# Kernel tuning notes

Hardware: AMD Instinct MI355X
Metric: run time of the kernel (lower is better)

The kernel has to match this reference:

```python
import jax, jax.numpy as jnp
import numpy as np

N_NODES = 100000


def gcn_conv(x, edge_index, W, b, n):
    """PyG GCNConv: h = x @ W; add self-loops; symmetric deg^-1/2 norm; scatter-add; + bias."""
    h = x @ W  # [N, out] -- transform first (PyG order), small message dim
    src, dst = edge_index[0], edge_index[1]
    loop = jnp.arange(n, dtype=src.dtype)
    src = jnp.concatenate([src, loop])
    dst = jnp.concatenate([dst, loop])
    # degree over targets with unit edge weights (includes self-loops)
    deg = jax.ops.segment_sum(jnp.ones_like(src, dtype=h.dtype), dst, num_segments=n)
    dinv = jnp.where(deg > 0, deg ** -0.5, 0.0)
    norm = dinv[src] * dinv[dst]  # [E+N]
    msg = h[src] * norm[:, None]  # gather + scale
    out = jax.ops.segment_sum(msg, dst, num_segments=n)  # scatter-add aggregate
    return out + b


def setup_inputs() -> dict:
    key = jax.random.key(0)
    k1, k2, k3, k4, k5, k6 = jax.random.split(key, 6)
    input_dim, hidden_dim, output_dim = 128, 16, 2
    x = jax.random.normal(k1, (N_NODES, input_dim), dtype=jnp.float32)
    edge_index = jax.random.randint(k2, (2, 3200000), 0, N_NODES, dtype=jnp.int64)
    s1 = (1.0 / np.sqrt(input_dim)).astype(np.float32)
    s2 = (1.0 / np.sqrt(hidden_dim)).astype(np.float32)
    W1 = jax.random.normal(k3, (input_dim, hidden_dim), dtype=jnp.float32) * s1
    b1 = jnp.zeros((hidden_dim,), dtype=jnp.float32)
    W2 = jax.random.normal(k4, (hidden_dim, output_dim), dtype=jnp.float32) * s2
    b2 = jnp.zeros((output_dim,), dtype=jnp.float32)
    return {"x": x, "edge_index": edge_index, "W1": W1, "b1": b1, "W2": W2, "b2": b2}


def reference(x, edge_index, W1, b1, W2, b2):
    n = x.shape[0]
    h = gcn_conv(x, edge_index, W1, b1, n)
    h = jax.nn.relu(h)
    out = gcn_conv(h, edge_index, W2, b2, n)
    return out
```

## Files before the change

### kernel.cpp

```cpp
#include <hip/hip_runtime.h>
#include <hip/hip_fp16.h>
#include <math.h>

constexpr int F_IN   = 128;
constexpr int F_H    = 16;
constexpr int F_OUT  = 2;
constexpr int BSH    = 8;
constexpr int BNODES = 1 << BSH;
constexpr int MAXB   = 512;
constexpr int BIN_SPAN = 8192;
constexpr int CAP    = 12288;

__global__ __launch_bounds__(256) void bcount_kernel(const int* __restrict__ dst, int E,
                                                     int* __restrict__ bcnt, int NB) {
    __shared__ int h[MAXB];
    for (int i = threadIdx.x; i < MAXB; i += 256) h[i] = 0;
    __syncthreads();
    int stride = gridDim.x * 256;
    for (int e = blockIdx.x * 256 + threadIdx.x; e < E; e += stride)
        atomicAdd(&h[dst[e] >> BSH], 1);
    __syncthreads();
    for (int b = threadIdx.x; b < NB; b += 256) {
        int c = h[b];
        if (c) atomicAdd(&bcnt[b], c);
    }
}

__global__ __launch_bounds__(256) void bscan_kernel(const int* __restrict__ bcnt,
                                                    int* __restrict__ boff,
                                                    int* __restrict__ gcur, int NB, int E) {
    __shared__ int warp_s[4];
    int t = threadIdx.x;
    int base = t * 4;
    int v0 = (base + 0 < NB) ? bcnt[base + 0] : 0;
    int v1 = (base + 1 < NB) ? bcnt[base + 1] : 0;
    int v2 = (base + 2 < NB) ? bcnt[base + 2] : 0;
    int v3 = (base + 3 < NB) ? bcnt[base + 3] : 0;
    int tsum = v0 + v1 + v2 + v3;
    int lane = t & 63, wid = t >> 6;
    int x = tsum;
    for (int d = 1; d < 64; d <<= 1) {
        int y = __shfl_up(x, d, 64);
        if (lane >= d) x += y;
    }
    if (lane == 63) warp_s[wid] = x;
    __syncthreads();
    if (t == 0) {
        int a = 0;
        for (int w = 0; w < 4; ++w) { int s = warp_s[w]; warp_s[w] = a; a += s; }
    }
    __syncthreads();
    int excl = x - tsum + warp_s[wid];
    int p0 = excl, p1 = excl + v0, p2 = excl + v0 + v1, p3 = excl + v0 + v1 + v2;
    if (base + 0 < NB) { boff[base + 0] = p0; gcur[base + 0] = p0; }
    if (base + 1 < NB) { boff[base + 1] = p1; gcur[base + 1] = p1; }
    if (base + 2 < NB) { boff[base + 2] = p2; gcur[base + 2] = p2; }
    if (base + 3 < NB) { boff[base + 3] = p3; gcur[base + 3] = p3; }
    if (t == 0) boff[NB] = E;
}

__global__ __launch_bounds__(1024) void bin_kernel(const int* __restrict__ src,
                                                   const int* __restrict__ dst,
                                                   int* __restrict__ gcur,
                                                   int* __restrict__ ebuf, int E) {
    __shared__ int cnt[MAXB];
    __shared__ int loff[MAXB];
    __shared__ int gbase[MAXB];
    __shared__ int warp_s[MAXB / 64];
    __shared__ int stagep[BIN_SPAN];
    __shared__ unsigned short stageb[BIN_SPAN];
    int tid = threadIdx.x;
    for (int i = tid; i < MAXB; i += 1024) cnt[i] = 0;
    __syncthreads();
    int e0 = blockIdx.x * BIN_SPAN;
    int e1 = min(e0 + BIN_SPAN, E);
    int m = e1 - e0;
    for (int i = tid; i < m; i += 1024)
        atomicAdd(&cnt[dst[e0 + i] >> BSH], 1);
    __syncthreads();
    int v = 0, x = 0;
    int lane = tid & 63, wid = tid >> 6;
    if (tid < MAXB) {
        v = cnt[tid];
        x = v;
        for (int d = 1; d < 64; d <<= 1) {
            int y = __shfl_up(x, d, 64);
            if (lane >= d) x += y;
        }
        if (lane == 63) warp_s[wid] = x;
    }
    __syncthreads();
    if (tid == 0) {
        int a = 0;
        for (int w = 0; w < MAXB / 64; ++w) { int s = warp_s[w]; warp_s[w] = a; a += s; }
    }
    __syncthreads();
    if (tid < MAXB) {
        int lo = x - v + warp_s[wid];
        loff[tid] = lo;
        gbase[tid] = (v ? atomicAdd(&gcur[tid], v) : 0) - lo;
        cnt[tid] = 0;
    }
    __syncthreads();
    for (int i = tid; i < m; i += 1024) {
        int d = dst[e0 + i];
        int b = d >> BSH;
        int r = atomicAdd(&cnt[b], 1);
        int idx = loff[b] + r;
        stagep[idx] = src[e0 + i] | ((d & (BNODES - 1)) << 17);
        stageb[idx] = (unsigned short)b;
    }
    __syncthreads();
    for (int i = tid; i < m; i += 1024)
        ebuf[gbase[stageb[i]] + i] = stagep[i];
}

__global__ __launch_bounds__(512) void csc_kernel(const int* __restrict__ boff,
                                                  int* __restrict__ ebuf,
                                                  float* __restrict__ dinv,
                                                  int* __restrict__ noff, int N) {
    __shared__ int stage[CAP];
    __shared__ int cnt[BNODES];
    __shared__ int loff[BNODES];
    __shared__ int cur[BNODES];
    int tid = threadIdx.x;
    int b = blockIdx.x;
    if (tid < BNODES) cnt[tid] = 0;
    __syncthreads();
    int e0 = boff[b], e1 = boff[b + 1];
    int m = min(e1 - e0, CAP);
    for (int i = tid; i < m; i += 512) {
        int v = ebuf[e0 + i];
        stage[i] = v;
        atomicAdd(&cnt[v >> 17], 1);
    }
    __syncthreads();
    if (tid == 0) {
        int a = 0;
        for (int j = 0; j < BNODES; ++j) { loff[j] = a; a += cnt[j]; }
    }
    __syncthreads();
    int n0 = b << BSH;
    if (tid < BNODES) {
        int node = n0 + tid;
        if (node < N) {
            dinv[node] = 1.0f / sqrtf((float)(cnt[tid] + 1));
            noff[node] = e0 + loff[tid];
        }
        cur[tid] = loff[tid];
    }
    if (tid == 0 && b == gridDim.x - 1) noff[N] = e1;
    __syncthreads();
    for (int i = tid; i < m; i += 512) {
        int v = stage[i];
        int p = atomicAdd(&cur[v >> 17], 1);
        ebuf[e0 + p] = v & 0x1FFFF;
    }
}

__global__ void gemm1_kernel(const float* __restrict__ x, const float* __restrict__ W1,
                             const float* __restrict__ dinv, __half* __restrict__ g1, int N) {
    __shared__ float w[F_IN * F_H];
    for (int t = threadIdx.x; t < F_IN * F_H; t += blockDim.x) w[t] = W1[t];
    __syncthreads();
    int row = blockIdx.x * blockDim.x + threadIdx.x;
    if (row >= N) return;
    float acc[F_H];
#pragma unroll
    for (int j = 0; j < F_H; ++j) acc[j] = 0.0f;
    const float4* xr = (const float4*)(x + (size_t)row * F_IN);
#pragma unroll 4
    for (int k4 = 0; k4 < F_IN / 4; ++k4) {
        float4 v = xr[k4];
        const float* wr = &w[k4 * 4 * F_H];
#pragma unroll
        for (int j = 0; j < F_H; ++j)
            acc[j] += v.x * wr[j] + v.y * wr[F_H + j] + v.z * wr[2 * F_H + j] + v.w * wr[3 * F_H + j];
    }
    float di = dinv[row];
    __half2 hh[8];
#pragma unroll
    for (int j = 0; j < 8; ++j)
        hh[j] = __floats2half2_rn(acc[2 * j] * di, acc[2 * j + 1] * di);
    uint4* gr = (uint4*)(g1 + (size_t)row * F_H);
    gr[0] = ((uint4*)hh)[0];
    gr[1] = ((uint4*)hh)[1];
}

__global__ __launch_bounds__(512) void agg1_kernel(
        const int* __restrict__ noff, const int* __restrict__ ebuf,
        const float* __restrict__ dinv, const __half2* __restrict__ g1,
        const float* __restrict__ b1, const float* __restrict__ W2,
        float* __restrict__ g2, int N) {
    int t = blockIdx.x * 512 + threadIdx.x;
    int node = t >> 3, lane = t & 7;
    if (node >= N) return;
    int k = noff[node], end = noff[node + 1];
    float2 a0 = make_float2(0.f, 0.f), a1 = a0, a2 = a0, a3 = a0;
    for (; k + 8 <= end; k += 8) {
        int s0 = ebuf[k + 0], s1 = ebuf[k + 1];
        int s2 = ebuf[k + 2], s3 = ebuf[k + 3];
        int s4 = ebuf[k + 4], s5 = ebuf[k + 5];
        int s6 = ebuf[k + 6], s7 = ebuf[k + 7];
        float2 v0 = __half22float2(g1[(s0 << 3) + lane]);
        float2 v1 = __half22float2(g1[(s1 << 3) + lane]);
        float2 v2 = __half22float2(g1[(s2 << 3) + lane]);
        float2 v3 = __half22float2(g1[(s3 << 3) + lane]);
        float2 v4 = __half22float2(g1[(s4 << 3) + lane]);
        float2 v5 = __half22float2(g1[(s5 << 3) + lane]);
        float2 v6 = __half22float2(g1[(s6 << 3) + lane]);
        float2 v7 = __half22float2(g1[(s7 << 3) + lane]);
        a0.x += v0.x; a0.y += v0.y;  a1.x += v1.x; a1.y += v1.y;
        a2.x += v2.x; a2.y += v2.y;  a3.x += v3.x; a3.y += v3.y;
        a0.x += v4.x; a0.y += v4.y;  a1.x += v5.x; a1.y += v5.y;
        a2.x += v6.x; a2.y += v6.y;  a3.x += v7.x; a3.y += v7.y;
    }
    for (; k < end; ++k) {
        float2 v = __half22float2(g1[(ebuf[k] << 3) + lane]);
        a0.x += v.x; a0.y += v.y;
    }
    float di = dinv[node];
    float2 sf = __half22float2(g1[(node << 3) + lane]);
    float sx = (a0.x + a1.x) + (a2.x + a3.x) + sf.x;
    float sy = (a0.y + a1.y) + (a2.y + a3.y) + sf.y;
    int j0 = 2 * lane, j1 = 2 * lane + 1;
    float yx = fmaxf(di * sx + b1[j0], 0.0f);
    float yy = fmaxf(di * sy + b1[j1], 0.0f);
    float o0 = yx * W2[j0 * F_OUT + 0] + yy * W2[j1 * F_OUT + 0];
    float o1 = yx * W2[j0 * F_OUT + 1] + yy * W2[j1 * F_OUT + 1];
#pragma unroll
    for (int d = 1; d < 8; d <<= 1) {
        o0 += __shfl_xor(o0, d, 64);
        o1 += __shfl_xor(o1, d, 64);
    }
    if (lane == 0) ((float2*)g2)[node] = make_float2(o0 * di, o1 * di);
}

__global__ __launch_bounds__(256) void agg2_kernel(
        const int* __restrict__ noff, const int* __restrict__ ebuf,
        const float* __restrict__ dinv, const float* __restrict__ g2,
        const float* __restrict__ b2, float* __restrict__ out, int N) {
    int t = blockIdx.x * 256 + threadIdx.x;
    int node = t >> 4, lane = t & 15;
    if (node >= N) return;
    int beg = noff[node], end = noff[node + 1];
    float a0 = 0.0f, a1 = 0.0f;
    for (int k = beg + lane; k < end; k += 16) {
        int s = ebuf[k];
        float2 g = ((const float2*)g2)[s];
        a0 += g.x; a1 += g.y;
    }
#pragma unroll
    for (int d = 1; d < 16; d <<= 1) {
        a0 += __shfl_xor(a0, d, 64);
        a1 += __shfl_xor(a1, d, 64);
    }
    if (lane == 0) {
        float di = dinv[node];
        float2 gs = ((const float2*)g2)[node];
        out[(size_t)node * F_OUT + 0] = b2[0] + di * (a0 + gs.x);
        out[(size_t)node * F_OUT + 1] = b2[1] + di * (a1 + gs.y);
    }
}

extern "C" void kernel_launch(void* const* d_in, const int* in_sizes, int n_in,
                              void* d_out, int out_size, void* d_ws, size_t ws_size,
                              hipStream_t stream) {
    const float* x  = (const float*)d_in[0];
    const int*   ei = (const int*)d_in[1];
    const float* W1 = (const float*)d_in[2];
    const float* b1 = (const float*)d_in[3];
    const float* W2 = (const float*)d_in[4];
    const float* b2 = (const float*)d_in[5];
    float* out = (float*)d_out;

    const int N = out_size / F_OUT;
    const int E = in_sizes[1] / 2;
    const int* srcp = ei;
    const int* dstp = ei + E;
    const int NB = (N + BNODES - 1) >> BSH;

    int* wsw = (int*)d_ws;
    size_t o = 0;
    int*    bcnt = wsw + o;  o += MAXB;
    int*    boff = wsw + o;  o += MAXB + 1;    o = (o + 3) & ~(size_t)3;
    int*    gcur = wsw + o;  o += MAXB;
    float*  dinv = (float*)(wsw + o);  o += (size_t)N;      o = (o + 3) & ~(size_t)3;
    int*    noff = wsw + o;  o += (size_t)N + 1;            o = (o + 3) & ~(size_t)3;
    int*    ebuf = wsw + o;  o += (size_t)E;                o = (o + 3) & ~(size_t)3;
    __half* g1h  = (__half*)(wsw + o); o += (size_t)N * F_H / 2;
    float*  g2   = (float*)(wsw + o);  o += (size_t)N * F_OUT;
    (void)ws_size;

    hipMemsetAsync(bcnt, 0, (size_t)NB * sizeof(int), stream);

    bcount_kernel<<<256, 256, 0, stream>>>(dstp, E, bcnt, NB);
    bscan_kernel<<<1, 256, 0, stream>>>(bcnt, boff, gcur, NB, E);
    bin_kernel<<<(E + BIN_SPAN - 1) / BIN_SPAN, 1024, 0, stream>>>(srcp, dstp, gcur, ebuf, E);
    csc_kernel<<<NB, 512, 0, stream>>>(boff, ebuf, dinv, noff, N);
    gemm1_kernel<<<(N + 255) / 256, 256, 0, stream>>>(x, W1, dinv, g1h, N);
    agg1_kernel<<<((size_t)N * 8 + 511) / 512, 512, 0, stream>>>(noff, ebuf, dinv,
                                                                 (const __half2*)g1h, b1, W2, g2, N);
    agg2_kernel<<<((size_t)N * 16 + 255) / 256, 256, 0, stream>>>(noff, ebuf, dinv, g2, b2, out, N);
}
```

Before: 229.3 us.

## Replace bucket count and scan passes with fixed-capacity bucket slots

Measured after the change: 203.7 us. 11.2% less time.

```diff
diff --git a/kernel.cpp b/kernel.cpp
--- a/kernel.cpp
+++ b/kernel.cpp
@@ -9,54 +9,11 @@
 constexpr int BNODES = 1 << BSH;
 constexpr int MAXB   = 512;
 constexpr int BIN_SPAN = 8192;
-constexpr int CAP    = 12288;
-
-__global__ __launch_bounds__(256) void bcount_kernel(const int* __restrict__ dst, int E,
-                                                     int* __restrict__ bcnt, int NB) {
-    __shared__ int h[MAXB];
-    for (int i = threadIdx.x; i < MAXB; i += 256) h[i] = 0;
-    __syncthreads();
-    int stride = gridDim.x * 256;
-    for (int e = blockIdx.x * 256 + threadIdx.x; e < E; e += stride)
-        atomicAdd(&h[dst[e] >> BSH], 1);
-    __syncthreads();
-    for (int b = threadIdx.x; b < NB; b += 256) {
-        int c = h[b];
-        if (c) atomicAdd(&bcnt[b], c);
-    }
-}
-
-__global__ __launch_bounds__(256) void bscan_kernel(const int* __restrict__ bcnt,
-                                                    int* __restrict__ boff,
-                                                    int* __restrict__ gcur, int NB, int E) {
-    __shared__ int warp_s[4];
-    int t = threadIdx.x;
-    int base = t * 4;
-    int v0 = (base + 0 < NB) ? bcnt[base + 0] : 0;
-    int v1 = (base + 1 < NB) ? bcnt[base + 1] : 0;
-    int v2 = (base + 2 < NB) ? bcnt[base + 2] : 0;
-    int v3 = (base + 3 < NB) ? bcnt[base + 3] : 0;
-    int tsum = v0 + v1 + v2 + v3;
-    int lane = t & 63, wid = t >> 6;
-    int x = tsum;
-    for (int d = 1; d < 64; d <<= 1) {
-        int y = __shfl_up(x, d, 64);
-        if (lane >= d) x += y;
-    }
-    if (lane == 63) warp_s[wid] = x;
-    __syncthreads();
-    if (t == 0) {
-        int a = 0;
-        for (int w = 0; w < 4; ++w) { int s = warp_s[w]; warp_s[w] = a; a += s; }
-    }
-    __syncthreads();
-    int excl = x - tsum + warp_s[wid];
-    int p0 = excl, p1 = excl + v0, p2 = excl + v0 + v1, p3 = excl + v0 + v1 + v2;
-    if (base + 0 < NB) { boff[base + 0] = p0; gcur[base + 0] = p0; }
-    if (base + 1 < NB) { boff[base + 1] = p1; gcur[base + 1] = p1; }
-    if (base + 2 < NB) { boff[base + 2] = p2; gcur[base + 2] = p2; }
-    if (base + 3 < NB) { boff[base + 3] = p3; gcur[base + 3] = p3; }
-    if (t == 0) boff[NB] = E;
+constexpr int CAP10  = 9216;
+
+__global__ void binit_kernel(int* __restrict__ gcur) {
+    int b = blockIdx.x * 256 + threadIdx.x;
+    if (b < MAXB) gcur[b] = b * CAP10;
 }
 
 __global__ __launch_bounds__(1024) void bin_kernel(const int* __restrict__ src,
@@ -115,46 +72,59 @@
         ebuf[gbase[stageb[i]] + i] = stagep[i];
 }
 
-__global__ __launch_bounds__(512) void csc_kernel(const int* __restrict__ boff,
+__global__ __launch_bounds__(512) void csc_kernel(const int* __restrict__ gcur,
                                                   int* __restrict__ ebuf,
                                                   float* __restrict__ dinv,
-                                                  int* __restrict__ noff, int N) {
-    __shared__ int stage[CAP];
+                                                  int* __restrict__ noff,
+                                                  int* __restrict__ ndeg, int N) {
+    __shared__ int stage[CAP10];
     __shared__ int cnt[BNODES];
-    __shared__ int loff[BNODES];
     __shared__ int cur[BNODES];
+    __shared__ int wsum[BNODES / 64];
     int tid = threadIdx.x;
     int b = blockIdx.x;
     if (tid < BNODES) cnt[tid] = 0;
     __syncthreads();
-    int e0 = boff[b], e1 = boff[b + 1];
-    int m = min(e1 - e0, CAP);
+    int e0 = b * CAP10;
+    int m = min(gcur[b] - e0, CAP10);
     for (int i = tid; i < m; i += 512) {
         int v = ebuf[e0 + i];
         stage[i] = v;
         atomicAdd(&cnt[v >> 17], 1);
     }
     __syncthreads();
+    int v = 0, x = 0;
+    int lane = tid & 63, wid = tid >> 6;
+    if (tid < BNODES) {
+        v = cnt[tid];
+        x = v;
+        for (int d = 1; d < 64; d <<= 1) {
+            int y = __shfl_up(x, d, 64);
+            if (lane >= d) x += y;
+        }
+        if (lane == 63) wsum[wid] = x;
+    }
+    __syncthreads();
     if (tid == 0) {
         int a = 0;
-        for (int j = 0; j < BNODES; ++j) { loff[j] = a; a += cnt[j]; }
-    }
-    __syncthreads();
-    int n0 = b << BSH;
+        for (int w = 0; w < BNODES / 64; ++w) { int s = wsum[w]; wsum[w] = a; a += s; }
+    }
+    __syncthreads();
     if (tid < BNODES) {
-        int node = n0 + tid;
+        int lo = x - v + wsum[wid];
+        cur[tid] = lo;
+        int node = (b << BSH) + tid;
         if (node < N) {
-            dinv[node] = 1.0f / sqrtf((float)(cnt[tid] + 1));
-            noff[node] = e0 + loff[tid];
+            dinv[node] = 1.0f / sqrtf((float)(v + 1));
+            noff[node] = e0 + lo;
+            ndeg[node] = v;
         }
-        cur[tid] = loff[tid];
-    }
-    if (tid == 0 && b == gridDim.x - 1) noff[N] = e1;
+    }
     __syncthreads();
     for (int i = tid; i < m; i += 512) {
-        int v = stage[i];
-        int p = atomicAdd(&cur[v >> 17], 1);
-        ebuf[e0 + p] = v & 0x1FFFF;
+        int vv = stage[i];
+        int p = atomicAdd(&cur[vv >> 17], 1);
+        ebuf[e0 + p] = vv & 0x1FFFF;
     }
 }
 
@@ -188,14 +158,15 @@
 }
 
 __global__ __launch_bounds__(512) void agg1_kernel(
-        const int* __restrict__ noff, const int* __restrict__ ebuf,
+        const int* __restrict__ noff, const int* __restrict__ ndeg,
+        const int* __restrict__ ebuf,
         const float* __restrict__ dinv, const __half2* __restrict__ g1,
         const float* __restrict__ b1, const float* __restrict__ W2,
         float* __restrict__ g2, int N) {
     int t = blockIdx.x * 512 + threadIdx.x;
     int node = t >> 3, lane = t & 7;
     if (node >= N) return;
-    int k = noff[node], end = noff[node + 1];
+    int k = noff[node], end = k + ndeg[node];
     float2 a0 = make_float2(0.f, 0.f), a1 = a0, a2 = a0, a3 = a0;
     for (; k + 8 <= end; k += 8) {
         int s0 = ebuf[k + 0], s1 = ebuf[k + 1];
@@ -237,13 +208,14 @@
 }
 
 __global__ __launch_bounds__(256) void agg2_kernel(
-        const int* __restrict__ noff, const int* __restrict__ ebuf,
+        const int* __restrict__ noff, const int* __restrict__ ndeg,
+        const int* __restrict__ ebuf,
         const float* __restrict__ dinv, const float* __restrict__ g2,
         const float* __restrict__ b2, float* __restrict__ out, int N) {
     int t = blockIdx.x * 256 + threadIdx.x;
     int node = t >> 4, lane = t & 15;
     if (node >= N) return;
-    int beg = noff[node], end = noff[node + 1];
+    int beg = noff[node], end = beg + ndeg[node];
     float a0 = 0.0f, a1 = 0.0f;
     for (int k = beg + lane; k < end; k += 16) {
         int s = ebuf[k];
@@ -282,24 +254,20 @@
 
     int* wsw = (int*)d_ws;
     size_t o = 0;
-    int*    bcnt = wsw + o;  o += MAXB;
-    int*    boff = wsw + o;  o += MAXB + 1;    o = (o + 3) & ~(size_t)3;
     int*    gcur = wsw + o;  o += MAXB;
     float*  dinv = (float*)(wsw + o);  o += (size_t)N;      o = (o + 3) & ~(size_t)3;
-    int*    noff = wsw + o;  o += (size_t)N + 1;            o = (o + 3) & ~(size_t)3;
-    int*    ebuf = wsw + o;  o += (size_t)E;                o = (o + 3) & ~(size_t)3;
+    int*    noff = wsw + o;  o += (size_t)N;                o = (o + 3) & ~(size_t)3;
+    int*    ndeg = wsw + o;  o += (size_t)N;                o = (o + 3) & ~(size_t)3;
+    int*    ebuf = wsw + o;  o += (size_t)NB * CAP10;       o = (o + 3) & ~(size_t)3;
     __half* g1h  = (__half*)(wsw + o); o += (size_t)N * F_H / 2;
     float*  g2   = (float*)(wsw + o);  o += (size_t)N * F_OUT;
     (void)ws_size;
 
-    hipMemsetAsync(bcnt, 0, (size_t)NB * sizeof(int), stream);
-
-    bcount_kernel<<<256, 256, 0, stream>>>(dstp, E, bcnt, NB);
-    bscan_kernel<<<1, 256, 0, stream>>>(bcnt, boff, gcur, NB, E);
+    binit_kernel<<<(MAXB + 255) / 256, 256, 0, stream>>>(gcur);
     bin_kernel<<<(E + BIN_SPAN - 1) / BIN_SPAN, 1024, 0, stream>>>(srcp, dstp, gcur, ebuf, E);
-    csc_kernel<<<NB, 512, 0, stream>>>(boff, ebuf, dinv, noff, N);
+    csc_kernel<<<NB, 512, 0, stream>>>(gcur, ebuf, dinv, noff, ndeg, N);
     gemm1_kernel<<<(N + 255) / 256, 256, 0, stream>>>(x, W1, dinv, g1h, N);
-    agg1_kernel<<<((size_t)N * 8 + 511) / 512, 512, 0, stream>>>(noff, ebuf, dinv,
+    agg1_kernel<<<((size_t)N * 8 + 511) / 512, 512, 0, stream>>>(noff, ndeg, ebuf, dinv,
                                                                  (const __half2*)g1h, b1, W2, g2, N);
-    agg2_kernel<<<((size_t)N * 16 + 255) / 256, 256, 0, stream>>>(noff, ebuf, dinv, g2, b2, out, N);
-}
+    agg2_kernel<<<((size_t)N * 16 + 255) / 256, 256, 0, stream>>>(noff, ndeg, ebuf, dinv, g2, b2, out, N);
+}
```
